# Performance work log

Hardware: AMD Instinct MI355X
Metric: run time of the kernel (lower is better)

## Reference

```python
import jax, jax.numpy as jnp
from jax import lax
import numpy as np

D = 640
HID = 64
DROP_RATIO = 0.1
N_ITER = int(D * DROP_RATIO)  # 64
TEMP = 0.07
EPS = 1e-7


def setup_inputs() -> dict:
    key = jax.random.key(0)
    k_x, k_w1, k_b1, k_w2, k_b2 = jax.random.split(key, 5)
    B = 8192
    x = jax.random.normal(k_x, (B, D), dtype=jnp.float32)
    # torch Linear default init: U(-1/sqrt(fan_in), 1/sqrt(fan_in))
    lim1 = 1.0 / np.sqrt(D)
    lim2 = 1.0 / np.sqrt(HID)
    W1 = jax.random.uniform(k_w1, (D, HID), minval=-lim1, maxval=lim1, dtype=jnp.float32)
    b1 = jax.random.uniform(k_b1, (HID,), minval=-lim1, maxval=lim1, dtype=jnp.float32)
    W2 = jax.random.uniform(k_w2, (HID, D), minval=-lim2, maxval=lim2, dtype=jnp.float32)
    b2 = jax.random.uniform(k_b2, (D,), minval=-lim2, maxval=lim2, dtype=jnp.float32)
    return {"x": x, "W1": W1, "b1": b1, "W2": W2, "b2": b2}


def reference(x, W1, b1, W2, b2):
    # small MLP: 640 -> 64 -> relu -> 640
    h = jnp.maximum(x @ W1 + b1, 0.0) @ W2 + b2  # (B, 640)

    def step(hhat, _):
        m = 1.0 - hhat
        mhat = jnp.log(m + EPS)
        yhat = jax.nn.softmax((-h + mhat) / TEMP, axis=-1)
        return hhat + yhat * m, None

    hhat0 = jnp.zeros_like(h)
    hhat, _ = lax.scan(jax.checkpoint(step), hhat0, None, length=N_ITER)
    mask = 1.0 - hhat
    return mask * x
```

## Files before the change

### kernel.cpp

```cpp
#include <hip/hip_runtime.h>

#define D 640
#define HID 64
#define NITER 64
#define ROWS 4
#define BLOCK 256

typedef float v2f __attribute__((ext_vector_type(2)));

#define DPP_ADD_STEP(v, ctrl, rmask)                                          \
    v += __builtin_bit_cast(float, __builtin_amdgcn_update_dpp(               \
             0, __builtin_bit_cast(int, v), ctrl, rmask, 0xf, true))
#define DPP_MAX_STEP(v, ctrl, rmask)                                          \
    v = fmaxf(v, __builtin_bit_cast(float, __builtin_amdgcn_update_dpp(       \
             __builtin_bit_cast(int, v), __builtin_bit_cast(int, v),          \
             ctrl, rmask, 0xf, false)))

__device__ __forceinline__ float wave_sum_dpp(float v) {
    DPP_ADD_STEP(v, 0x111, 0xf);
    DPP_ADD_STEP(v, 0x112, 0xf);
    DPP_ADD_STEP(v, 0x114, 0xf);
    DPP_ADD_STEP(v, 0x118, 0xf);
    DPP_ADD_STEP(v, 0x142, 0xa);
    DPP_ADD_STEP(v, 0x143, 0xc);
    return __builtin_bit_cast(float,
        __builtin_amdgcn_readlane(__builtin_bit_cast(int, v), 63));
}
__device__ __forceinline__ float wave_max_dpp(float v) {
    DPP_MAX_STEP(v, 0x111, 0xf);
    DPP_MAX_STEP(v, 0x112, 0xf);
    DPP_MAX_STEP(v, 0x114, 0xf);
    DPP_MAX_STEP(v, 0x118, 0xf);
    DPP_MAX_STEP(v, 0x142, 0xa);
    DPP_MAX_STEP(v, 0x143, 0xc);
    return __builtin_bit_cast(float,
        __builtin_amdgcn_readlane(__builtin_bit_cast(int, v), 63));
}

__global__ __launch_bounds__(BLOCK, 8) void dimmask_kernel(
    const float* __restrict__ x, const float* __restrict__ W1,
    const float* __restrict__ b1, const float* __restrict__ W2,
    const float* __restrict__ b2, float* __restrict__ out)
{
    constexpr float INV_T = 1.0f / 0.07f;
    constexpr float LOG2E = 1.4426950408889634f;
    constexpr float TEMP  = 0.07f;

    __shared__ float lds_a[ROWS][D];
    __shared__ float lds_part[4][ROWS][HID];
    __shared__ float lds_hid[ROWS][HID];

    const int tid  = threadIdx.x;
    const int row0 = blockIdx.x * ROWS;

    {
        const float4* xv  = (const float4*)(x + (size_t)row0 * D);
        float4*       lxv = (float4*)(&lds_a[0][0]);
        for (int i = tid; i < ROWS * D / 4; i += BLOCK) lxv[i] = xv[i];
    }
    __syncthreads();

    {
        const int k = tid & 63, c = tid >> 6;
        float acc[ROWS] = {0.f, 0.f, 0.f, 0.f};
        const int q0 = c * 40;
#pragma unroll 4
        for (int q = q0; q < q0 + 40; ++q) {
            const int tb = q * 4;
            float w0 = W1[(tb + 0) * HID + k];
            float w1 = W1[(tb + 1) * HID + k];
            float w2 = W1[(tb + 2) * HID + k];
            float w3 = W1[(tb + 3) * HID + k];
#pragma unroll
            for (int r = 0; r < ROWS; ++r) {
                float4 xa = ((const float4*)&lds_a[r][0])[q];
                acc[r] += xa.x * w0 + xa.y * w1 + xa.z * w2 + xa.w * w3;
            }
        }
#pragma unroll
        for (int r = 0; r < ROWS; ++r) lds_part[c][r][k] = acc[r];
    }
    __syncthreads();
    {
        const int r = tid >> 6, k = tid & 63;
        float s = lds_part[0][r][k] + lds_part[1][r][k]
                + lds_part[2][r][k] + lds_part[3][r][k] + b1[k];
        lds_hid[r][k] = fmaxf(s, 0.f);
    }
    __syncthreads();

    for (int j = tid; j < D; j += BLOCK) {
        float acc[ROWS] = {0.f, 0.f, 0.f, 0.f};
#pragma unroll 4
        for (int k4 = 0; k4 < HID / 4; ++k4) {
            const int kb = k4 * 4;
            float w0 = W2[(kb + 0) * D + j];
            float w1 = W2[(kb + 1) * D + j];
            float w2 = W2[(kb + 2) * D + j];
            float w3 = W2[(kb + 3) * D + j];
#pragma unroll
            for (int r = 0; r < ROWS; ++r) {
                float4 hh = ((const float4*)&lds_hid[r][0])[k4];
                acc[r] += hh.x * w0 + hh.y * w1 + hh.z * w2 + hh.w * w3;
            }
        }
        float bb = b2[j];
#pragma unroll
        for (int r = 0; r < ROWS; ++r)
            lds_a[r][j] = -(acc[r] + bb) * (LOG2E * INV_T);
    }
    __syncthreads();

    const int r = tid >> 6, l = tid & 63;
    v2f e2[5];
    float hmax;
    {
        float ht[10];
        hmax = -3.0e38f;
#pragma unroll
        for (int u = 0; u < 10; ++u) {
            ht[u] = lds_a[r][l + 64 * u];
            hmax = fmaxf(hmax, ht[u]);
        }
        hmax = wave_max_dpp(hmax);
#pragma unroll
        for (int u = 0; u < 5; ++u) {
            e2[u].x = __builtin_amdgcn_exp2f(fmaxf(ht[2 * u]     - hmax, -80.f));
            e2[u].y = __builtin_amdgcn_exp2f(fmaxf(ht[2 * u + 1] - hmax, -80.f));
        }
    }

    const v2f K1 = {1.0f, 1.0f};
    const v2f P4 = {-0.0395668f, -0.0395668f};
    const v2f P3 = {-0.0583090f, -0.0583090f};
    const v2f P2 = {-0.1020408f, -0.1020408f};
    const v2f P1 = {-0.2857143f, -0.2857143f};

    v2f sacc = (e2[0] + e2[1]) + ((e2[2] + e2[3]) + e2[4]);

    for (int it = 0; it < NITER; ++it) {
        float s  = wave_sum_dpp(sacc.x + sacc.y);
        float rs = __builtin_amdgcn_rcpf(s);
        float a = -14.2857143f * rs;
        float b = (94.8979592f * rs) * rs;
        float thr = 0.02f * s;
        v2f av = {a, a}, bv = {b, b};
        v2f ns = {0.f, 0.f};
#pragma unroll
        for (int u = 0; u < 5; ++u) {
            v2f e = e2[u];
            if (__builtin_expect(__any(fmaxf(e.x, e.y) > thr), 0)) {
                v2f y  = e * rs;
                v2f f  = K1 - y;
                v2f f2 = f * f, f4 = f2 * f2, f8 = f4 * f4;
                v2f f14 = f8 * f4 * f2;
                v2f p = __builtin_elementwise_fma(P4, y, P3);
                p = __builtin_elementwise_fma(p, y, P2);
                p = __builtin_elementwise_fma(p, y, P1);
                p = __builtin_elementwise_fma(p, y, K1);
                e *= f14 * p;
            } else {
                v2f p = __builtin_elementwise_fma(bv, e, av);
                p = __builtin_elementwise_fma(p, e, K1);
                e *= p;
            }
            e2[u] = e;
            ns += e;
        }
        sacc = ns;
    }

    const float* xrow = x + (size_t)(row0 + r) * D;
    float* orow = out + (size_t)(row0 + r) * D;
#pragma unroll
    for (int u = 0; u < 5; ++u) {
        const int j0 = l + 128 * u, j1 = j0 + 64;
        float c0 = fmaxf(lds_a[r][j0] - hmax, -80.f);
        float c1 = fmaxf(lds_a[r][j1] - hmax, -80.f);
        float m0 = __builtin_amdgcn_exp2f(TEMP * (__builtin_amdgcn_logf(e2[u].x) - c0));
        float m1 = __builtin_amdgcn_exp2f(TEMP * (__builtin_amdgcn_logf(e2[u].y) - c1));
        orow[j0] = m0 * xrow[j0];
        orow[j1] = m1 * xrow[j1];
    }
}

extern "C" void kernel_launch(void* const* d_in, const int* in_sizes, int n_in,
                              void* d_out, int out_size, void* d_ws, size_t ws_size,
                              hipStream_t stream) {
    const float* x  = (const float*)d_in[0];
    const float* W1 = (const float*)d_in[1];
    const float* b1 = (const float*)d_in[2];
    const float* W2 = (const float*)d_in[3];
    const float* b2 = (const float*)d_in[4];
    float* out = (float*)d_out;

    const int B = in_sizes[0] / D;
    dim3 grid(B / ROWS), block(BLOCK);
    hipLaunchKernelGGL(dimmask_kernel, grid, block, 0, stream, x, W1, b1, W2, b2, out);
}
```

Before: 177.8 us.

## Process two rows per wave to interleave independent reduction chains

Doubles rows per block from 4 to 8, so each wave now runs the 64-iteration softmax-mask recurrence for two rows at once. The two rows' DPP reductions and elementwise updates are interleaved, which hides the latency of the serial reduce-then-update chain and halves the number of blocks. The MLP stages reuse each W1/W2 load across twice as many rows. In exchange, register and LDS use per block roughly double, the launch bound drops to 4 blocks per CU, and the per-row divergent-branch checks are duplicated.

```diff
diff --git a/kernel.cpp b/kernel.cpp
--- a/kernel.cpp
+++ b/kernel.cpp
@@ -3,7 +3,7 @@
 #define D 640
 #define HID 64
 #define NITER 64
-#define ROWS 4
+#define ROWS 8
 #define BLOCK 256
 
 typedef float v2f __attribute__((ext_vector_type(2)));
@@ -16,28 +16,61 @@
              __builtin_bit_cast(int, v), __builtin_bit_cast(int, v),          \
              ctrl, rmask, 0xf, false)))
 
-__device__ __forceinline__ float wave_sum_dpp(float v) {
-    DPP_ADD_STEP(v, 0x111, 0xf);
-    DPP_ADD_STEP(v, 0x112, 0xf);
-    DPP_ADD_STEP(v, 0x114, 0xf);
-    DPP_ADD_STEP(v, 0x118, 0xf);
-    DPP_ADD_STEP(v, 0x142, 0xa);
-    DPP_ADD_STEP(v, 0x143, 0xc);
-    return __builtin_bit_cast(float,
-        __builtin_amdgcn_readlane(__builtin_bit_cast(int, v), 63));
-}
-__device__ __forceinline__ float wave_max_dpp(float v) {
-    DPP_MAX_STEP(v, 0x111, 0xf);
-    DPP_MAX_STEP(v, 0x112, 0xf);
-    DPP_MAX_STEP(v, 0x114, 0xf);
-    DPP_MAX_STEP(v, 0x118, 0xf);
-    DPP_MAX_STEP(v, 0x142, 0xa);
-    DPP_MAX_STEP(v, 0x143, 0xc);
-    return __builtin_bit_cast(float,
-        __builtin_amdgcn_readlane(__builtin_bit_cast(int, v), 63));
-}
-
-__global__ __launch_bounds__(BLOCK, 8) void dimmask_kernel(
+__device__ __forceinline__ void wave_sum_dpp2(float& a, float& b) {
+    DPP_ADD_STEP(a, 0x111, 0xf);  DPP_ADD_STEP(b, 0x111, 0xf);
+    DPP_ADD_STEP(a, 0x112, 0xf);  DPP_ADD_STEP(b, 0x112, 0xf);
+    DPP_ADD_STEP(a, 0x114, 0xf);  DPP_ADD_STEP(b, 0x114, 0xf);
+    DPP_ADD_STEP(a, 0x118, 0xf);  DPP_ADD_STEP(b, 0x118, 0xf);
+    DPP_ADD_STEP(a, 0x142, 0xa);  DPP_ADD_STEP(b, 0x142, 0xa);
+    DPP_ADD_STEP(a, 0x143, 0xc);  DPP_ADD_STEP(b, 0x143, 0xc);
+    a = __builtin_bit_cast(float,
+        __builtin_amdgcn_readlane(__builtin_bit_cast(int, a), 63));
+    b = __builtin_bit_cast(float,
+        __builtin_amdgcn_readlane(__builtin_bit_cast(int, b), 63));
+}
+__device__ __forceinline__ void wave_max_dpp2(float& a, float& b) {
+    DPP_MAX_STEP(a, 0x111, 0xf);  DPP_MAX_STEP(b, 0x111, 0xf);
+    DPP_MAX_STEP(a, 0x112, 0xf);  DPP_MAX_STEP(b, 0x112, 0xf);
+    DPP_MAX_STEP(a, 0x114, 0xf);  DPP_MAX_STEP(b, 0x114, 0xf);
+    DPP_MAX_STEP(a, 0x118, 0xf);  DPP_MAX_STEP(b, 0x118, 0xf);
+    DPP_MAX_STEP(a, 0x142, 0xa);  DPP_MAX_STEP(b, 0x142, 0xa);
+    DPP_MAX_STEP(a, 0x143, 0xc);  DPP_MAX_STEP(b, 0x143, 0xc);
+    a = __builtin_bit_cast(float,
+        __builtin_amdgcn_readlane(__builtin_bit_cast(int, a), 63));
+    b = __builtin_bit_cast(float,
+        __builtin_amdgcn_readlane(__builtin_bit_cast(int, b), 63));
+}
+
+__device__ __forceinline__ void unit_step(v2f& e2u, float rs, float a, float b,
+                                          float thr, v2f& ns) {
+    const v2f K1 = {1.0f, 1.0f};
+    const v2f P4 = {-0.0395668f, -0.0395668f};
+    const v2f P3 = {-0.0583090f, -0.0583090f};
+    const v2f P2 = {-0.1020408f, -0.1020408f};
+    const v2f P1 = {-0.2857143f, -0.2857143f};
+    v2f e = e2u;
+    if (__builtin_expect(__any(fmaxf(e.x, e.y) > thr), 0)) {
+        v2f rsv = {rs, rs};
+        v2f y  = e * rsv;
+        v2f f  = K1 - y;
+        v2f f2 = f * f, f4 = f2 * f2, f8 = f4 * f4;
+        v2f f14 = (f8 * f4) * f2;
+        v2f p = __builtin_elementwise_fma(P4, y, P3);
+        p = __builtin_elementwise_fma(p, y, P2);
+        p = __builtin_elementwise_fma(p, y, P1);
+        p = __builtin_elementwise_fma(p, y, K1);
+        e *= f14 * p;
+    } else {
+        v2f av = {a, a}, bv = {b, b};
+        v2f p = __builtin_elementwise_fma(bv, e, av);
+        p = __builtin_elementwise_fma(p, e, K1);
+        e *= p;
+    }
+    e2u = e;
+    ns += e;
+}
+
+__global__ __launch_bounds__(BLOCK, 4) void dimmask_kernel(
     const float* __restrict__ x, const float* __restrict__ W1,
     const float* __restrict__ b1, const float* __restrict__ W2,
     const float* __restrict__ b2, float* __restrict__ out)
@@ -62,9 +95,11 @@
 
     {
         const int k = tid & 63, c = tid >> 6;
-        float acc[ROWS] = {0.f, 0.f, 0.f, 0.f};
+        float acc[ROWS];
+#pragma unroll
+        for (int r = 0; r < ROWS; ++r) acc[r] = 0.f;
         const int q0 = c * 40;
-#pragma unroll 4
+#pragma unroll 2
         for (int q = q0; q < q0 + 40; ++q) {
             const int tb = q * 4;
             float w0 = W1[(tb + 0) * HID + k];
@@ -81,8 +116,8 @@
         for (int r = 0; r < ROWS; ++r) lds_part[c][r][k] = acc[r];
     }
     __syncthreads();
-    {
-        const int r = tid >> 6, k = tid & 63;
+    for (int idx = tid; idx < ROWS * HID; idx += BLOCK) {
+        const int r = idx >> 6, k = idx & 63;
         float s = lds_part[0][r][k] + lds_part[1][r][k]
                 + lds_part[2][r][k] + lds_part[3][r][k] + b1[k];
         lds_hid[r][k] = fmaxf(s, 0.f);
@@ -90,8 +125,10 @@
     __syncthreads();
 
     for (int j = tid; j < D; j += BLOCK) {
-        float acc[ROWS] = {0.f, 0.f, 0.f, 0.f};
-#pragma unroll 4
+        float acc[ROWS];
+#pragma unroll
+        for (int r = 0; r < ROWS; ++r) acc[r] = 0.f;
+#pragma unroll 2
         for (int k4 = 0; k4 < HID / 4; ++k4) {
             const int kb = k4 * 4;
             float w0 = W2[(kb + 0) * D + j];
@@ -111,76 +148,71 @@
     }
     __syncthreads();
 
-    const int r = tid >> 6, l = tid & 63;
-    v2f e2[5];
-    float hmax;
+    const int w = tid >> 6, l = tid & 63;
+    const int rA = 2 * w, rB = 2 * w + 1;
+    v2f eA[5], eB[5];
+    float hmaxA, hmaxB;
     {
-        float ht[10];
-        hmax = -3.0e38f;
+        float htA[10], htB[10];
+        float ha = -3.0e38f, hb = -3.0e38f;
 #pragma unroll
         for (int u = 0; u < 10; ++u) {
-            ht[u] = lds_a[r][l + 64 * u];
-            hmax = fmaxf(hmax, ht[u]);
-        }
-        hmax = wave_max_dpp(hmax);
+            htA[u] = lds_a[rA][l + 64 * u];
+            htB[u] = lds_a[rB][l + 64 * u];
+            ha = fmaxf(ha, htA[u]);
+            hb = fmaxf(hb, htB[u]);
+        }
+        wave_max_dpp2(ha, hb);
+        hmaxA = ha; hmaxB = hb;
 #pragma unroll
         for (int u = 0; u < 5; ++u) {
-            e2[u].x = __builtin_amdgcn_exp2f(fmaxf(ht[2 * u]     - hmax, -80.f));
-            e2[u].y = __builtin_amdgcn_exp2f(fmaxf(ht[2 * u + 1] - hmax, -80.f));
-        }
-    }
-
-    const v2f K1 = {1.0f, 1.0f};
-    const v2f P4 = {-0.0395668f, -0.0395668f};
-    const v2f P3 = {-0.0583090f, -0.0583090f};
-    const v2f P2 = {-0.1020408f, -0.1020408f};
-    const v2f P1 = {-0.2857143f, -0.2857143f};
-
-    v2f sacc = (e2[0] + e2[1]) + ((e2[2] + e2[3]) + e2[4]);
+            eA[u].x = __builtin_amdgcn_exp2f(fmaxf(htA[2 * u]     - ha, -80.f));
+            eA[u].y = __builtin_amdgcn_exp2f(fmaxf(htA[2 * u + 1] - ha, -80.f));
+            eB[u].x = __builtin_amdgcn_exp2f(fmaxf(htB[2 * u]     - hb, -80.f));
+            eB[u].y = __builtin_amdgcn_exp2f(fmaxf(htB[2 * u + 1] - hb, -80.f));
+        }
+    }
+
+    v2f saccA = (eA[0] + eA[1]) + ((eA[2] + eA[3]) + eA[4]);
+    v2f saccB = (eB[0] + eB[1]) + ((eB[2] + eB[3]) + eB[4]);
 
     for (int it = 0; it < NITER; ++it) {
-        float s  = wave_sum_dpp(sacc.x + sacc.y);
-        float rs = __builtin_amdgcn_rcpf(s);
-        float a = -14.2857143f * rs;
-        float b = (94.8979592f * rs) * rs;
-        float thr = 0.02f * s;
-        v2f av = {a, a}, bv = {b, b};
-        v2f ns = {0.f, 0.f};
+        float sA = saccA.x + saccA.y;
+        float sB = saccB.x + saccB.y;
+        wave_sum_dpp2(sA, sB);
+        float rsA = __builtin_amdgcn_rcpf(sA);
+        float rsB = __builtin_amdgcn_rcpf(sB);
+        float aA = -14.2857143f * rsA, bA = (94.8979592f * rsA) * rsA;
+        float aB = -14.2857143f * rsB, bB = (94.8979592f * rsB) * rsB;
+        float thrA = 0.02f * sA, thrB = 0.02f * sB;
+        v2f nsA = {0.f, 0.f}, nsB = {0.f, 0.f};
 #pragma unroll
         for (int u = 0; u < 5; ++u) {
-            v2f e = e2[u];
-            if (__builtin_expect(__any(fmaxf(e.x, e.y) > thr), 0)) {
-                v2f y  = e * rs;
-                v2f f  = K1 - y;
-                v2f f2 = f * f, f4 = f2 * f2, f8 = f4 * f4;
-                v2f f14 = f8 * f4 * f2;
-                v2f p = __builtin_elementwise_fma(P4, y, P3);
-                p = __builtin_elementwise_fma(p, y, P2);
-                p = __builtin_elementwise_fma(p, y, P1);
-                p = __builtin_elementwise_fma(p, y, K1);
-                e *= f14 * p;
-            } else {
-                v2f p = __builtin_elementwise_fma(bv, e, av);
-                p = __builtin_elementwise_fma(p, e, K1);
-                e *= p;
-            }
-            e2[u] = e;
-            ns += e;
-        }
-        sacc = ns;
-    }
-
-    const float* xrow = x + (size_t)(row0 + r) * D;
-    float* orow = out + (size_t)(row0 + r) * D;
-#pragma unroll
-    for (int u = 0; u < 5; ++u) {
-        const int j0 = l + 128 * u, j1 = j0 + 64;
-        float c0 = fmaxf(lds_a[r][j0] - hmax, -80.f);
-        float c1 = fmaxf(lds_a[r][j1] - hmax, -80.f);
-        float m0 = __builtin_amdgcn_exp2f(TEMP * (__builtin_amdgcn_logf(e2[u].x) - c0));
-        float m1 = __builtin_amdgcn_exp2f(TEMP * (__builtin_amdgcn_logf(e2[u].y) - c1));
-        orow[j0] = m0 * xrow[j0];
-        orow[j1] = m1 * xrow[j1];
+            unit_step(eA[u], rsA, aA, bA, thrA, nsA);
+            unit_step(eB[u], rsB, aB, bB, thrB, nsB);
+        }
+        saccA = nsA; saccB = nsB;
+    }
+
+#pragma unroll
+    for (int pr = 0; pr < 2; ++pr) {
+        const int r = (pr == 0) ? rA : rB;
+        const float hm = (pr == 0) ? hmaxA : hmaxB;
+        v2f* e2 = (pr == 0) ? eA : eB;
+        const float* xrow = x + (size_t)(row0 + r) * D;
+        float* orow = out + (size_t)(row0 + r) * D;
+#pragma unroll
+        for (int u = 0; u < 5; ++u) {
+            const int j0 = l + 128 * u, j1 = j0 + 64;
+            float c0 = fmaxf(lds_a[r][j0] - hm, -80.f);
+            float c1 = fmaxf(lds_a[r][j1] - hm, -80.f);
+            float m0 = __builtin_amdgcn_exp2f(
+                TEMP * (__builtin_amdgcn_logf(e2[u].x) - c0));
+            float m1 = __builtin_amdgcn_exp2f(
+                TEMP * (__builtin_amdgcn_logf(e2[u].y) - c1));
+            orow[j0] = m0 * xrow[j0];
+            orow[j1] = m1 * xrow[j1];
+        }
     }
 }
 
```

After: 182.9 us. +2.9%, slower.
